# Performance work log

Measured on AMD Instinct MI355X. Metric: run time of the kernel, lower is better.

The kernel has to match this reference:

```python
import jax, jax.numpy as jnp
import numpy as np

B, S = 1024, 512
V, E, H, T = 50000, 300, 800, 50


def setup_inputs() -> dict:
    key = jax.random.key(0)
    ks = jax.random.split(key, 8)
    ids = jax.random.randint(ks[0], (B, S), 0, V, dtype=jnp.int64 if jax.config.jax_enable_x64 else jnp.int32)
    return {
        "ids": ids,
        "rho": jax.random.normal(ks[1], (V, E), jnp.float32) * 0.02,
        "alpha": jax.random.normal(ks[2], (T, E), jnp.float32) * 0.02,
        "W1": jax.random.normal(ks[3], (E, H), jnp.float32) * 0.05,
        "b1": jnp.zeros((H,), jnp.float32),
        "Wmu": jax.random.normal(ks[4], (H, T), jnp.float32) * 0.05,
        "bmu": jnp.zeros((T,), jnp.float32),
        "Wlv": jax.random.normal(ks[5], (H, T), jnp.float32) * 0.05,
        "blv": jnp.zeros((T,), jnp.float32),
    }


def reference(ids, rho, alpha, W1, b1, Wmu, bmu, Wlv, blv):
    b, s = ids.shape
    v = rho.shape[0]
    # bag-of-words histogram: scatter-add instead of dense one_hot+reduce_sum
    bows = jnp.zeros((b, v), rho.dtype).at[jnp.arange(b)[:, None], ids].add(1.0)
    # zero out special tokens 1 and 2 (original: x * (1 - sum(one_hot([1,2]))))
    bows = bows.at[:, jnp.array([1, 2])].set(0.0)
    normal_bows = bows / jnp.sum(bows, axis=-1, keepdims=True)
    # encoder (eval mode: dropout is identity)
    x = jnp.einsum('bv,ve->be', normal_bows, rho)
    h = jax.nn.relu(x @ W1 + b1)
    mu_theta = h @ Wmu + bmu
    logsigma_theta = h @ Wlv + blv
    kl_theta = -0.5 * jnp.sum(1.0 + logsigma_theta - mu_theta**2 - jnp.exp(logsigma_theta), axis=-1)
    # reparameterize (eval/inference mode): z = mu
    theta = jax.nn.softmax(mu_theta, axis=-1)  # [B, T]
    beta = jax.nn.softmax(jnp.einsum('te,ve->tv', alpha, rho), axis=-1)  # [T, V]
    lookup = jnp.log(theta @ beta + 1e-5)  # [B, V]
    recon_loss = -jnp.sum(lookup * bows, axis=-1)
    loss = jnp.mean(recon_loss) + jnp.mean(kl_theta)
    return theta, loss
```

## Files before the change

kernel.cpp:

```cpp
#include <hip/hip_runtime.h>
#include <math.h>


#define Bn 1024
#define Sn 512
#define Vn 50000
#define En 300
#define Hn 800
#define Tn 50
#define KP 320
#define BSTR 64
#define W1FRAG_N (50 * 10 * 64 * 8)
#define WFRAG_N  (8 * 25 * 64 * 8)
#define NRANGE 8
#define VRANGE (Vn / NRANGE)
#define CASTB 7813
#define K4B (Vn / 16)

typedef __bf16 bf16x8 __attribute__((ext_vector_type(8)));
typedef float  f32x4  __attribute__((ext_vector_type(4)));
typedef float  f32x2  __attribute__((ext_vector_type(2)));

__device__ __forceinline__ float waveReduceSum(float v) {
    #pragma unroll
    for (int off = 32; off > 0; off >>= 1) v += __shfl_xor(v, off, 64);
    return v;
}
__device__ __forceinline__ float waveReduceMax(float v) {
    #pragma unroll
    for (int off = 32; off > 0; off >>= 1) v = fmaxf(v, __shfl_xor(v, off, 64));
    return v;
}
__device__ __forceinline__ unsigned short f2bf(float x) {
    unsigned u = __float_as_uint(x);
    return (unsigned short)((u + 0x7FFFu + ((u >> 16) & 1u)) >> 16);
}
__device__ __forceinline__ float bf_lo(unsigned u) { return __uint_as_float(u << 16); }
__device__ __forceinline__ float bf_hi(unsigned u) { return __uint_as_float(u & 0xFFFF0000u); }
__device__ __forceinline__ int lane_prefix(unsigned long long m) {
    return __builtin_amdgcn_mbcnt_hi((unsigned)(m >> 32),
           __builtin_amdgcn_mbcnt_lo((unsigned)m, 0));
}

#define PKACC(u) { \
    c0 += (f32x2){bf_lo((u).x), bf_hi((u).x)}; \
    c1 += (f32x2){bf_lo((u).y), bf_hi((u).y)}; \
    c2 += (f32x2){bf_lo((u).z), bf_hi((u).z)}; \
    c3 += (f32x2){bf_lo((u).w), bf_hi((u).w)}; }

__global__ __launch_bounds__(256) void ka_init(
        const float4* __restrict__ rho4, unsigned short* __restrict__ rhoh,
        const float* __restrict__ alpha, const float* __restrict__ W1,
        const float* __restrict__ Wmu, const float* __restrict__ Wlv,
        unsigned short* __restrict__ bfrag, unsigned short* __restrict__ w1frag,
        unsigned short* __restrict__ wfrag, float* __restrict__ topicsumR,
        float* __restrict__ loss) {
    if (blockIdx.x < CASTB) {
        const int i = blockIdx.x * 256 + threadIdx.x;
        if (i < Vn * (KP / 8)) {
            int v = i / (KP / 8), s8 = i - v * (KP / 8);
            int c = s8 * 8;
            ushort4 o0 = {0, 0, 0, 0}, o1 = {0, 0, 0, 0};
            if (c < En) {
                float4 r = rho4[v * (En / 4) + s8 * 2];
                o0.x = f2bf(r.x); o0.y = f2bf(r.y); o0.z = f2bf(r.z); o0.w = f2bf(r.w);
            }
            if (c + 4 < En) {
                float4 r = rho4[v * (En / 4) + s8 * 2 + 1];
                o1.x = f2bf(r.x); o1.y = f2bf(r.y); o1.z = f2bf(r.z); o1.w = f2bf(r.w);
            }
            uint4 st;
            st.x = (unsigned)o0.x | ((unsigned)o0.y << 16);
            st.y = (unsigned)o0.z | ((unsigned)o0.w << 16);
            st.z = (unsigned)o1.x | ((unsigned)o1.y << 16);
            st.w = (unsigned)o1.z | ((unsigned)o1.w << 16);
            *(uint4*)(rhoh + (size_t)v * KP + c) = st;
        }
        return;
    }
    const int gid = (blockIdx.x - CASTB) * 256 + threadIdx.x;
    if (gid < 512) topicsumR[gid] = 0.f;
    if (gid == 520) *loss = 0.f;
    if (gid < 4 * 10 * 64 * 8) {
        int j = gid & 7;
        int lane = (gid >> 3) & 63;
        int rest = gid >> 9;
        int kt = rest % 10, w = rest / 10;
        int t = 16 * w + (lane & 15);
        int e = kt * 32 + (lane >> 4) * 8 + j;
        bfrag[gid] = (t < Tn && e < En) ? f2bf(alpha[t * En + e]) : (unsigned short)0;
    }
    if (gid < W1FRAG_N) {
        int j = gid & 7, lane = (gid >> 3) & 63, rest = gid >> 9;
        int kt = rest % 10, nt = rest / 10;
        int e = kt * 32 + (lane >> 4) * 8 + j;
        int hcol = nt * 16 + (lane & 15);
        w1frag[gid] = (e < En) ? f2bf(W1[e * Hn + hcol]) : (unsigned short)0;
    } else {
        int g2 = gid - W1FRAG_N;
        if (g2 < WFRAG_N) {
            int j = g2 & 7, lane = (g2 >> 3) & 63, rest = g2 >> 9;
            int kt = rest % 25, nt = rest / 25;
            int k = kt * 32 + (lane >> 4) * 8 + j;
            int t = (nt & 3) * 16 + (lane & 15);
            float val = 0.f;
            if (t < Tn) val = (nt < 4) ? Wmu[k * Tn + t] : Wlv[k * Tn + t];
            wfrag[g2] = f2bf(val);
        }
    }
}

__global__ __launch_bounds__(256) void kb_beta_tokens(
        const unsigned short* __restrict__ rhoh,
        const unsigned short* __restrict__ bfrag,
        unsigned int* __restrict__ betaU32, float* __restrict__ topicsumR,
        const int* __restrict__ ids, int* __restrict__ toks,
        int* __restrict__ cnt, float* __restrict__ xbarP) {
    __shared__ unsigned short trans[16 * 66];
    __shared__ __align__(16) int sid[Sn];
    __shared__ int sfid[Sn];
    __shared__ __align__(16) float xred[4][320];
    __shared__ int scount, sfull;
    const int tid = threadIdx.x;
    const int wave = tid >> 6, lane = tid & 63;

    if (blockIdx.x < K4B) {
        const int quad = lane >> 4, l15 = lane & 15;
        const int v0 = blockIdx.x * 16;
        const unsigned short* arow = rhoh + (size_t)(v0 + l15) * KP + quad * 8;
        f32x4 acc = {0.f, 0.f, 0.f, 0.f};
        #pragma unroll
        for (int kt = 0; kt < 10; ++kt) {
            bf16x8 a = *(const bf16x8*)(arow + kt * 32);
            bf16x8 bv = *(const bf16x8*)(bfrag + ((wave * 10 + kt) * 64 + lane) * 8);
            acc = __builtin_amdgcn_mfma_f32_16x16x32_bf16(a, bv, acc, 0, 0, 0);
        }
        float ts = 0.f;
        #pragma unroll
        for (int r = 0; r < 4; ++r) {
            float ev = expf(acc[r]);
            ts += ev;
            trans[(quad * 4 + r) * 66 + 16 * wave + l15] = f2bf(ev);
        }
        ts += __shfl_xor(ts, 16, 64);
        ts += __shfl_xor(ts, 32, 64);
        const int t = 16 * wave + l15;
        if (lane < 16 && t < Tn)
            atomicAdd(&topicsumR[(blockIdx.x & 7) * 64 + t], ts);
        __syncthreads();
        unsigned int* dst = betaU32 + (size_t)v0 * 32;
        const unsigned int* tr32 = (const unsigned int*)trans;
        for (int i = tid; i < 16 * 32; i += 256)
            dst[i] = tr32[(i >> 5) * 33 + (i & 31)];
        return;
    }
    const int blk = blockIdx.x - K4B;
    const int r = blk & (NRANGE - 1), b = blk >> 3;
    const int lo = r * VRANGE, hi = lo + VRANGE;
    if (tid == 0) { scount = 0; sfull = 0; }
    __syncthreads();
    #pragma unroll
    for (int s0 = 0; s0 < Sn; s0 += 256) {
        int id = ids[b * Sn + s0 + tid];
        bool val = (id != 1 && id != 2);
        bool inr = val && id >= lo && id < hi;
        unsigned long long mb = __ballot(inr);
        int pre = lane_prefix(mb);
        int wc = __popcll(mb);
        int base = 0;
        if (lane == 0 && wc) base = atomicAdd(&scount, wc);
        base = __shfl(base, 0, 64);
        if (inr) sid[base + pre] = id;
        if (r == 0) {
            unsigned long long fb = __ballot(val);
            int fpre = lane_prefix(fb);
            int fwc = __popcll(fb);
            int fbase = 0;
            if (lane == 0 && fwc) fbase = atomicAdd(&sfull, fwc);
            fbase = __shfl(fbase, 0, 64);
            if (val) sfid[fbase + fpre] = id;
        }
    }
    __syncthreads();
    if (r == 0) {
        const int nf = sfull;
        for (int i = tid; i < nf; i += 256) toks[b * Sn + i] = sfid[i];
        if (tid == 0) cnt[b] = nf;
    }
    const int m = scount;
    f32x2 c0 = {0.f, 0.f}, c1 = {0.f, 0.f}, c2 = {0.f, 0.f}, c3 = {0.f, 0.f};
    if (m > 0 && lane < 40) {
        const uint4* rb = (const uint4*)rhoh;
        const int mm1 = m - 1;
        int s = wave;
        #define LDT(S) rb[(size_t)sid[(S) < mm1 ? (S) : mm1] * 40 + lane]
        uint4 p0 = LDT(s), p1 = LDT(s + 4), p2 = LDT(s + 8), p3 = LDT(s + 12);
        for (; s < m; s += 16) {
            uint4 n0 = LDT(s + 16), n1 = LDT(s + 20),
                  n2 = LDT(s + 24), n3 = LDT(s + 28);
            __builtin_amdgcn_sched_barrier(0);
            PKACC(p0);
            if (s + 4 < m)  PKACC(p1);
            if (s + 8 < m)  PKACC(p2);
            if (s + 12 < m) PKACC(p3);
            p0 = n0; p1 = n1; p2 = n2; p3 = n3;
        }
        #undef LDT
        float* xw = &xred[wave][lane * 8];
        *(float4*)(xw)     = (float4){c0[0], c0[1], c1[0], c1[1]};
        *(float4*)(xw + 4) = (float4){c2[0], c2[1], c3[0], c3[1]};
    } else if (lane < 40) {
        float* xw = &xred[wave][lane * 8];
        *(float4*)(xw)     = (float4){0.f, 0.f, 0.f, 0.f};
        *(float4*)(xw + 4) = (float4){0.f, 0.f, 0.f, 0.f};
    }
    __syncthreads();
    float* xbp = xbarP + ((size_t)b * NRANGE + r) * KP;
    for (int c = tid; c < KP; c += 256)
        xbp[c] = xred[0][c] + xred[1][c] + xred[2][c] + xred[3][c];
}

__global__ __launch_bounds__(256) void kx_norm(
        const float* __restrict__ xbarP, const int* __restrict__ cnt,
        unsigned short* __restrict__ xsg) {
    const int i = blockIdx.x * 256 + threadIdx.x;
    const int b = i / (KP / 4), e4 = (i - b * (KP / 4)) * 4;
    const float in = 1.0f / (float)cnt[b];
    const float* bp = xbarP + ((size_t)b * NRANGE) * KP + e4;
    float sx = 0.f, sy = 0.f, sz = 0.f, sw_ = 0.f;
    #pragma unroll
    for (int rr = 0; rr < NRANGE; ++rr) {
        float4 v = *(const float4*)(bp + rr * KP);
        sx += v.x; sy += v.y; sz += v.z; sw_ += v.w;
    }
    ushort4 o;
    o.x = f2bf(sx * in); o.y = f2bf(sy * in);
    o.z = f2bf(sz * in); o.w = f2bf(sw_ * in);
    *(ushort4*)&xsg[(size_t)b * KP + e4] = o;
}

__global__ __launch_bounds__(256) void k2m_h(
        const unsigned short* __restrict__ xsg,
        const unsigned short* __restrict__ w1frag,
        const float* __restrict__ b1, unsigned short* __restrict__ hbh) {
    __shared__ unsigned short xs[16 * 328];
    const int tid = threadIdx.x;
    const int wave = tid >> 6, lane = tid & 63;
    const int quad = lane >> 4, l15 = lane & 15;
    const int b0 = blockIdx.x * 16;
    for (int i = tid; i < 16 * (KP / 8); i += 256) {
        int row = i / (KP / 8), e8 = (i - row * (KP / 8)) * 8;
        *(uint4*)&xs[row * 328 + e8] = *(const uint4*)&xsg[(size_t)(b0 + row) * KP + e8];
    }
    __syncthreads();
    const int nt = blockIdx.y * 4 + wave;
    if (nt < 50) {
        const unsigned short* arow = xs + l15 * 328 + quad * 8;
        f32x4 acc = {0.f, 0.f, 0.f, 0.f};
        #pragma unroll
        for (int kt = 0; kt < 10; ++kt) {
            bf16x8 a = *(const bf16x8*)(arow + kt * 32);
            bf16x8 bv = *(const bf16x8*)(w1frag + ((size_t)(nt * 10 + kt) * 64 + lane) * 8);
            acc = __builtin_amdgcn_mfma_f32_16x16x32_bf16(a, bv, acc, 0, 0, 0);
        }
        const int col = nt * 16 + l15;
        const float bias = b1[col];
        #pragma unroll
        for (int r = 0; r < 4; ++r) {
            int row = b0 + quad * 4 + r;
            hbh[(size_t)row * Hn + col] = f2bf(fmaxf(acc[r] + bias, 0.f));
        }
    }
}

__global__ __launch_bounds__(256) void k3_theta(
        const unsigned short* __restrict__ hbh,
        const unsigned short* __restrict__ wfrag,
        const float* __restrict__ bmu, const float* __restrict__ blv,
        float* __restrict__ theta, float* __restrict__ loss) {
    __shared__ float mlds[16 * 65];
    __shared__ float llds[16 * 65];
    const int tid = threadIdx.x;
    const int wave = tid >> 6, lane = tid & 63;
    const int quad = lane >> 4, l15 = lane & 15;
    const int b0 = blockIdx.x * 16;
    const unsigned short* arow = hbh + (size_t)(b0 + l15) * Hn + quad * 8;
    f32x4 am = {0.f, 0.f, 0.f, 0.f}, al = {0.f, 0.f, 0.f, 0.f};
    #pragma unroll
    for (int kt = 0; kt < 25; ++kt) {
        bf16x8 a  = *(const bf16x8*)(arow + kt * 32);
        bf16x8 bm = *(const bf16x8*)(wfrag + ((size_t)(wave * 25 + kt) * 64 + lane) * 8);
        bf16x8 bl = *(const bf16x8*)(wfrag + ((size_t)((4 + wave) * 25 + kt) * 64 + lane) * 8);
        am = __builtin_amdgcn_mfma_f32_16x16x32_bf16(a, bm, am, 0, 0, 0);
        al = __builtin_amdgcn_mfma_f32_16x16x32_bf16(a, bl, al, 0, 0, 0);
    }
    const int t = wave * 16 + l15;
    const float bm_ = (t < Tn) ? bmu[t] : 0.f;
    const float bl_ = (t < Tn) ? blv[t] : 0.f;
    #pragma unroll
    for (int r = 0; r < 4; ++r) {
        int row = quad * 4 + r;
        mlds[row * 65 + t] = am[r] + bm_;
        llds[row * 65 + t] = al[r] + bl_;
    }
    __syncthreads();
    const int tt = (lane < Tn) ? lane : (Tn - 1);
    const bool act = (lane < Tn);
    float klacc = 0.f;
    #pragma unroll
    for (int k = 0; k < 4; ++k) {
        int row = wave * 4 + k;
        float mu = mlds[row * 65 + tt];
        float lv = llds[row * 65 + tt];
        float m = waveReduceMax(act ? mu : -1e30f);
        float ex = act ? expf(mu - m) : 0.f;
        float ssum = waveReduceSum(ex);
        if (act) theta[(b0 + row) * Tn + lane] = ex / ssum;
        klacc += waveReduceSum(act ? (1.f + lv - mu * mu - expf(lv)) : 0.f);
    }
    if (lane == 0) atomicAdd(loss, -0.5f * klacc * (1.0f / (float)Bn));
}

__global__ __launch_bounds__(256) void k6_recon(
        const int* __restrict__ toks, const int* __restrict__ cnt,
        const float* __restrict__ theta, const float* __restrict__ topicsumR,
        const unsigned short* __restrict__ betaUh, float* __restrict__ loss) {
    __shared__ float sw[Tn];
    __shared__ float swred[4];
    const int b = blockIdx.x, tid = threadIdx.x;
    if (tid < Tn) {
        float z = 0.f;
        #pragma unroll
        for (int j = 0; j < 8; ++j) z += topicsumR[j * 64 + tid];
        sw[tid] = theta[b * Tn + tid] / z;
    }
    __syncthreads();
    float wr[Tn];
    #pragma unroll
    for (int t = 0; t < Tn; ++t) wr[t] = sw[t];
    float lsum = 0.f;
    const int n = cnt[b];
    for (int i = tid; i < n; i += 256) {
        int v = toks[b * Sn + i];
        const uint4* q = (const uint4*)(betaUh + (size_t)v * BSTR);
        float dot = 0.f;
        #pragma unroll
        for (int k = 0; k < 6; ++k) {
            uint4 u = q[k];
            int t = 8 * k;
            dot += wr[t]     * bf_lo(u.x) + wr[t + 1] * bf_hi(u.x);
            dot += wr[t + 2] * bf_lo(u.y) + wr[t + 3] * bf_hi(u.y);
            dot += wr[t + 4] * bf_lo(u.z) + wr[t + 5] * bf_hi(u.z);
            dot += wr[t + 6] * bf_lo(u.w) + wr[t + 7] * bf_hi(u.w);
        }
        unsigned d = ((const unsigned*)q)[24];
        dot += wr[48] * bf_lo(d) + wr[49] * bf_hi(d);
        lsum += logf(dot + 1e-5f);
    }
    float s = waveReduceSum(lsum);
    const int wave = tid >> 6, lane = tid & 63;
    if (lane == 0) swred[wave] = s;
    __syncthreads();
    if (tid == 0) {
        float tot = swred[0] + swred[1] + swred[2] + swred[3];
        atomicAdd(loss, -tot * (1.0f / (float)Bn));
    }
}

extern "C" void kernel_launch(void* const* d_in, const int* in_sizes, int n_in,
                              void* d_out, int out_size, void* d_ws, size_t ws_size,
                              hipStream_t stream) {
    const int*   ids   = (const int*)d_in[0];
    const float* rho   = (const float*)d_in[1];
    const float* alpha = (const float*)d_in[2];
    const float* W1    = (const float*)d_in[3];
    const float* b1    = (const float*)d_in[4];
    const float* Wmu   = (const float*)d_in[5];
    const float* bmu   = (const float*)d_in[6];
    const float* Wlv   = (const float*)d_in[7];
    const float* blv   = (const float*)d_in[8];

    float* theta = (float*)d_out;
    float* loss  = theta + Bn * Tn;

    char* w = (char*)d_ws;
    float* topicsumR = (float*)w;               w += 8 * 64 * 4;
    unsigned short* bfrag = (unsigned short*)w; w += 4 * 10 * 64 * 8 * 2;
    unsigned short* w1frag = (unsigned short*)w; w += (size_t)W1FRAG_N * 2;
    unsigned short* wfrag = (unsigned short*)w;  w += (size_t)WFRAG_N * 2;
    int*   cnt      = (int*)w;                  w += Bn * 4;
    int*   toks     = (int*)w;                  w += Bn * Sn * 4;
    float* xbarP    = (float*)w;                w += (size_t)Bn * NRANGE * KP * 4;
    unsigned short* hbh = (unsigned short*)w;   w += (size_t)Bn * Hn * 2;
    unsigned short* rhoh = (unsigned short*)w;  w += (size_t)Vn * KP * 2;
    unsigned int* betaU32 = (unsigned int*)w;   w += (size_t)Vn * 128;
    unsigned short* xsg = (unsigned short*)w;   w += (size_t)Bn * KP * 2;

    const int k0grid = (W1FRAG_N + WFRAG_N + 255) / 256;
    ka_init<<<CASTB + k0grid, 256, 0, stream>>>(
        (const float4*)rho, rhoh, alpha, W1, Wmu, Wlv,
        bfrag, w1frag, wfrag, topicsumR, loss);
    kb_beta_tokens<<<K4B + Bn * NRANGE, 256, 0, stream>>>(
        rhoh, bfrag, betaU32, topicsumR, ids, toks, cnt, xbarP);
    kx_norm<<<Bn * (KP / 4) / 256, 256, 0, stream>>>(xbarP, cnt, xsg);
    k2m_h<<<dim3(64, 13), 256, 0, stream>>>(xsg, w1frag, b1, hbh);
    k3_theta<<<64, 256, 0, stream>>>(hbh, wfrag, bmu, blv, theta, loss);
    k6_recon<<<Bn, 256, 0, stream>>>(toks, cnt, theta, topicsumR,
                                     (const unsigned short*)betaU32, loss);
}
```

Before: 201.5 us.

## Align vocab ranges to beta tiles and software-pipeline rho gathers with inline asm

The beta-tile blocks are remapped so each group of eight blocks covers a contiguous 16-row-aligned vocabulary range, and the token-range split uses the same boundaries. The rho gather loop now uses inline-asm global loads with double-buffered register sets and explicit vmcnt waits, so the loads for the next group are in flight while the current one is accumulated. This is meant to hide gather latency and keep beta and token ranges aligned. In exchange it adds some idle blocks that return early, and correctness depends on the hand-written waitcnt ordering being right.

```diff
diff --git a/kernel.cpp b/kernel.cpp
--- a/kernel.cpp
+++ b/kernel.cpp
@@ -13,9 +13,8 @@
 #define W1FRAG_N (50 * 10 * 64 * 8)
 #define WFRAG_N  (8 * 25 * 64 * 8)
 #define NRANGE 8
-#define VRANGE (Vn / NRANGE)
 #define CASTB 7813
-#define K4B (Vn / 16)
+#define K4B 3128
 
 typedef __bf16 bf16x8 __attribute__((ext_vector_type(8)));
 typedef float  f32x4  __attribute__((ext_vector_type(4)));
@@ -40,6 +39,9 @@
 __device__ __forceinline__ int lane_prefix(unsigned long long m) {
     return __builtin_amdgcn_mbcnt_hi((unsigned)(m >> 32),
            __builtin_amdgcn_mbcnt_lo((unsigned)m, 0));
+}
+__device__ __forceinline__ void gload16a(uint4& d, const uint4* a) {
+    asm volatile("global_load_dwordx4 %0, %1, off" : "=v"(d) : "v"(a));
 }
 
 #define PKACC(u) { \
@@ -125,8 +127,12 @@
     const int wave = tid >> 6, lane = tid & 63;
 
     if (blockIdx.x < K4B) {
+        const int x = blockIdx.x & 7;
+        const int n = blockIdx.x >> 3;
+        const int tile = ((x * 3125) >> 3) + n;
+        if (tile >= (((x + 1) * 3125) >> 3)) return;
         const int quad = lane >> 4, l15 = lane & 15;
-        const int v0 = blockIdx.x * 16;
+        const int v0 = tile * 16;
         const unsigned short* arow = rhoh + (size_t)(v0 + l15) * KP + quad * 8;
         f32x4 acc = {0.f, 0.f, 0.f, 0.f};
         #pragma unroll
@@ -146,7 +152,7 @@
         ts += __shfl_xor(ts, 32, 64);
         const int t = 16 * wave + l15;
         if (lane < 16 && t < Tn)
-            atomicAdd(&topicsumR[(blockIdx.x & 7) * 64 + t], ts);
+            atomicAdd(&topicsumR[x * 64 + t], ts);
         __syncthreads();
         unsigned int* dst = betaU32 + (size_t)v0 * 32;
         const unsigned int* tr32 = (const unsigned int*)trans;
@@ -156,7 +162,8 @@
     }
     const int blk = blockIdx.x - K4B;
     const int r = blk & (NRANGE - 1), b = blk >> 3;
-    const int lo = r * VRANGE, hi = lo + VRANGE;
+    const int lo = ((r * 3125) >> 3) * 16;
+    const int hi = (((r + 1) * 3125) >> 3) * 16;
     if (tid == 0) { scount = 0; sfull = 0; }
     __syncthreads();
     #pragma unroll
@@ -192,27 +199,39 @@
     if (m > 0 && lane < 40) {
         const uint4* rb = (const uint4*)rhoh;
         const int mm1 = m - 1;
+        uint4 A0, A1, A2, A3, B0, B1, B2, B3;
+        #define ADDR(S) (rb + (size_t)sid[(S) < mm1 ? (S) : mm1] * 40 + lane)
         int s = wave;
-        #define LDT(S) rb[(size_t)sid[(S) < mm1 ? (S) : mm1] * 40 + lane]
-        uint4 p0 = LDT(s), p1 = LDT(s + 4), p2 = LDT(s + 8), p3 = LDT(s + 12);
-        for (; s < m; s += 16) {
-            uint4 n0 = LDT(s + 16), n1 = LDT(s + 20),
-                  n2 = LDT(s + 24), n3 = LDT(s + 28);
+        gload16a(A0, ADDR(s));      gload16a(A1, ADDR(s + 4));
+        gload16a(A2, ADDR(s + 8));  gload16a(A3, ADDR(s + 12));
+        for (;;) {
+            gload16a(B0, ADDR(s + 16)); gload16a(B1, ADDR(s + 20));
+            gload16a(B2, ADDR(s + 24)); gload16a(B3, ADDR(s + 28));
+            asm volatile("s_waitcnt vmcnt(4)" ::: "memory");
             __builtin_amdgcn_sched_barrier(0);
-            PKACC(p0);
-            if (s + 4 < m)  PKACC(p1);
-            if (s + 8 < m)  PKACC(p2);
-            if (s + 12 < m) PKACC(p3);
-            p0 = n0; p1 = n1; p2 = n2; p3 = n3;
-        }
-        #undef LDT
+            if (s < m)      PKACC(A0);
+            if (s + 4 < m)  PKACC(A1);
+            if (s + 8 < m)  PKACC(A2);
+            if (s + 12 < m) PKACC(A3);
+            s += 16;
+            if (s >= m) break;
+            gload16a(A0, ADDR(s + 16)); gload16a(A1, ADDR(s + 20));
+            gload16a(A2, ADDR(s + 24)); gload16a(A3, ADDR(s + 28));
+            asm volatile("s_waitcnt vmcnt(4)" ::: "memory");
+            __builtin_amdgcn_sched_barrier(0);
+            if (s < m)      PKACC(B0);
+            if (s + 4 < m)  PKACC(B1);
+            if (s + 8 < m)  PKACC(B2);
+            if (s + 12 < m) PKACC(B3);
+            s += 16;
+            if (s >= m) break;
+        }
+        #undef ADDR
+    }
+    if (lane < 40) {
         float* xw = &xred[wave][lane * 8];
         *(float4*)(xw)     = (float4){c0[0], c0[1], c1[0], c1[1]};
         *(float4*)(xw + 4) = (float4){c2[0], c2[1], c3[0], c3[1]};
-    } else if (lane < 40) {
-        float* xw = &xred[wave][lane * 8];
-        *(float4*)(xw)     = (float4){0.f, 0.f, 0.f, 0.f};
-        *(float4*)(xw + 4) = (float4){0.f, 0.f, 0.f, 0.f};
     }
     __syncthreads();
     float* xbp = xbarP + ((size_t)b * NRANGE + r) * KP;
```

After: 200.0 us. Within noise of the previous version (-0.8%).
